# Performance work log

Hardware: AMD Instinct MI355X
Metric: run time of the kernel (lower is better)

## Reference

```python
import jax, jax.numpy as jnp
import numpy as np

EPS = 1e-06
K = 32


def setup_inputs() -> dict:
    key = jax.random.key(0)
    k1, k2, k3, k4, k5 = jax.random.split(key, 5)
    d_model, n_latents = 1024, 16384
    x = jax.random.normal(k1, (2, 2048, d_model), dtype=jnp.float32)
    b_pre = jax.random.normal(k2, (d_model,), dtype=jnp.float32) * 0.02
    W_enc = jax.random.normal(k3, (n_latents, d_model), dtype=jnp.float32) / np.sqrt(d_model)
    b_enc = jax.random.normal(k4, (n_latents,), dtype=jnp.float32) * 0.02
    W_dec = jax.random.normal(k5, (d_model, n_latents), dtype=jnp.float32)
    # mimic normalize_decoder_weights: unit norm along dim=1 (n_latents axis per row)
    W_dec = W_dec / jnp.linalg.norm(W_dec, axis=1, keepdims=True)
    return {"x": x, "b_pre": b_pre, "W_enc": W_enc, "b_enc": b_enc, "W_dec": W_dec}


def reference(x, b_pre, W_enc, b_enc, W_dec):
    B, S, D = x.shape
    # preprocess: center + normalize (torch .std is unbiased, ddof=1)
    mean = jnp.mean(x, axis=-1, keepdims=True)
    norm = jnp.std(x, axis=-1, keepdims=True, ddof=1) + EPS
    xn = ((x - mean) / norm).reshape(-1, D)          # [N, D]
    # encode
    h = (xn - b_pre) @ W_enc.T + b_enc               # [N, n_latents]
    # top-k + relu + scatter into sparse latent
    vals, idx = jax.lax.top_k(h, K)                  # [N, K]
    vals = jax.nn.relu(vals)
    rows = jnp.arange(h.shape[0])[:, None]
    h_sparse = jnp.zeros_like(h).at[rows, idx].set(vals)
    # decode (dense matmul over mostly-zero latents, as in the original)
    recon = h_sparse @ W_dec.T + b_pre               # [N, D]
    # postprocess: denormalize
    recon = recon.reshape(B, S, D) * norm + mean
    return recon
```

## Files before the change

### kernel.cpp

```cpp
#include <hip/hip_runtime.h>
#include <cstdint>
#include <cstddef>

typedef _Float16 half_t;
typedef _Float16 half4_t __attribute__((ext_vector_type(4)));
typedef _Float16 half8_t __attribute__((ext_vector_type(8)));
typedef unsigned short ushort8_t __attribute__((ext_vector_type(8)));
typedef float floatx4 __attribute__((ext_vector_type(4)));

#define NROWS 4096
#define DMODEL 1024
#define NLAT 16384
#define CAND_MAX 256

#define MBYTE (1ull << 20)
static const size_t oW0    = 0;
static const size_t oWdT   = 32 * MBYTE;
static const size_t oMeanF = 64 * MBYTE;
static const size_t oNormF = 64 * MBYTE + (64ull << 10);
static const size_t oMeanD = 64 * MBYTE + (128ull << 10);
static const size_t oNormD = 64 * MBYTE + (192ull << 10);
static const size_t oCandC = 64 * MBYTE + (256ull << 10);
static const size_t oCandI = 65 * MBYTE;
static const size_t oCandV = 69 * MBYTE;
static const size_t oBatch = 77 * MBYTE;

#define BATCH_ROW_BYTES 34816ull

__device__ __forceinline__ void gload16(const void* g, void* l) {
  __builtin_amdgcn_global_load_lds(
      (const __attribute__((address_space(1))) void*)g,
      (__attribute__((address_space(3))) void*)l, 16, 0, 0);
}

__device__ __forceinline__ uint32_t okey16(uint32_t u) {
  return (u & 0x8000u) ? ((~u) & 0xFFFFu) : (u | 0x8000u);
}
__device__ __forceinline__ float inv_okey16(uint32_t k) {
  unsigned short u = (k & 0x8000u) ? (unsigned short)(k & 0x7FFFu)
                                   : (unsigned short)(~k);
  return (float)__builtin_bit_cast(_Float16, u);
}

#define WSPLIT_B 2048
#define TRANS_B  4096
__global__ __launch_bounds__(256) void prepro_kernel(
    const float* __restrict__ x, const float* __restrict__ b_pre,
    const float* __restrict__ W_enc, const float* __restrict__ Wd,
    half_t* __restrict__ W0h, half_t* __restrict__ WdT,
    half_t* __restrict__ X0,
    float* __restrict__ meanF, float* __restrict__ normF,
    double* __restrict__ meanD, double* __restrict__ normD, int r0) {
  int bid = blockIdx.x, tid = threadIdx.x;
  if (bid < WSPLIT_B) {
    size_t base = (size_t)bid * 2048 + tid;
    for (int it = 0; it < 8; ++it) {
      size_t i = base + (size_t)it * 256;
      float4 v = ((const float4*)W_enc)[i];
      half4_t h0;
      h0[0] = (half_t)(v.x * 1024.0f);
      h0[1] = (half_t)(v.y * 1024.0f);
      h0[2] = (half_t)(v.z * 1024.0f);
      h0[3] = (half_t)(v.w * 1024.0f);
      ((half4_t*)W0h)[i] = h0;
    }
    return;
  }
  if (bid < WSPLIT_B + TRANS_B) {
    __shared__ float tile[64][65];
    int t = bid - WSPLIT_B;
    int c0 = (t & 255) * 64;
    int r0t = (t >> 8) * 64;
    int tc = tid & 63, tg = tid >> 6;
    for (int i = 0; i < 16; ++i) {
      int rr = i * 4 + tg;
      tile[rr][tc] = Wd[(size_t)(r0t + rr) * NLAT + c0 + tc];
    }
    __syncthreads();
    for (int i = 0; i < 16; ++i) {
      int cc = i * 4 + tg;
      WdT[(size_t)(c0 + cc) * DMODEL + r0t + tc] = (half_t)tile[tc][cc];
    }
    return;
  }
  int rl = bid - WSPLIT_B - TRANS_B;
  int rg = r0 + rl;
  const float4* px = (const float4*)(x + (size_t)rg * DMODEL);
  float4 v = px[tid];
  double s  = (double)v.x + (double)v.y + (double)v.z + (double)v.w;
  double sq = (double)v.x * v.x + (double)v.y * v.y +
              (double)v.z * v.z + (double)v.w * v.w;
  for (int off = 32; off; off >>= 1) {
    s += __shfl_down(s, off);
    sq += __shfl_down(sq, off);
  }
  __shared__ double ss[4], ssq[4];
  __shared__ double sMean, sNorm;
  int wv = tid >> 6, ln = tid & 63;
  if (ln == 0) { ss[wv] = s; ssq[wv] = sq; }
  __syncthreads();
  if (tid == 0) {
    double S = ss[0] + ss[1] + ss[2] + ss[3];
    double Q = ssq[0] + ssq[1] + ssq[2] + ssq[3];
    double mean = S / (double)DMODEL;
    double var = (Q - (double)DMODEL * mean * mean) / (double)(DMODEL - 1);
    double nrm = sqrt(var) + 1e-6;
    sMean = mean; sNorm = nrm;
    meanF[rg] = (float)mean; normF[rg] = (float)nrm;
    meanD[rg] = mean;        normD[rg] = nrm;
  }
  __syncthreads();
  float mean = (float)sMean, nrm = (float)sNorm;
  const float4* pb = (const float4*)b_pre;
  float4 bp = pb[tid];
  float c[4];
  c[0] = ((v.x - mean) / nrm - bp.x) * 1024.0f;
  c[1] = ((v.y - mean) / nrm - bp.y) * 1024.0f;
  c[2] = ((v.z - mean) / nrm - bp.z) * 1024.0f;
  c[3] = ((v.w - mean) / nrm - bp.w) * 1024.0f;
  half4_t h0;
  for (int i = 0; i < 4; ++i) h0[i] = (half_t)c[i];
  ((half4_t*)(X0 + (size_t)rl * DMODEL))[tid] = h0;
}

__global__ __launch_bounds__(512, 2) void gemm_enc(
    const half_t* __restrict__ X0, const half_t* __restrict__ W0,
    const float* __restrict__ b_enc, half_t* __restrict__ h, int mtiles) {
  __shared__ __align__(16) half_t As[2][256 * 64];
  __shared__ __align__(16) half_t Bs[2][256 * 64];
  int tid = threadIdx.x;
  int lane = tid & 63, wave = tid >> 6;
  int wm = wave >> 2, wn = wave & 3;

  int bid = blockIdx.x;
  int xcd = bid & 7, q = bid >> 3;
  int bn = xcd * 8 + (q & 7);
  int bm = q >> 3;
  (void)mtiles;

  const char* Ag = (const char*)(X0 + (size_t)bm * 256 * DMODEL);
  const char* Bg = (const char*)(W0 + (size_t)bn * 256 * DMODEL);

  int srcSwz = ((lane & 7) ^ (lane >> 3)) << 4;
  int rowBase = wave * 8 + (lane >> 3);
  int ldsWOff = wave * 1024;

#define STG_A(b, kt, pr) { int colB = ((kt) & 15) * 128 + srcSwz;             \
    gload16(Ag + (size_t)((pr) * 64 + rowBase) * 2048 + colB,                 \
            (char*)As[b] + (pr) * 8192 + ldsWOff);                            \
    gload16(Ag + (size_t)(((pr) + 2) * 64 + rowBase) * 2048 + colB,           \
            (char*)As[b] + ((pr) + 2) * 8192 + ldsWOff); }
#define STG_B(b, kt, pr) { int colB = ((kt) & 15) * 128 + srcSwz;             \
    gload16(Bg + (size_t)((pr) * 64 + rowBase) * 2048 + colB,                 \
            (char*)Bs[b] + (pr) * 8192 + ldsWOff);                            \
    gload16(Bg + (size_t)(((pr) + 2) * 64 + rowBase) * 2048 + colB,           \
            (char*)Bs[b] + ((pr) + 2) * 8192 + ldsWOff); }

  floatx4 acc[8][4] = {};

  STG_B(0, 0, 0); STG_B(0, 0, 1); STG_A(0, 0, 0); STG_A(0, 0, 1);
  STG_B(1, 1, 0); STG_B(1, 1, 1); STG_A(1, 1, 0);
  asm volatile("s_waitcnt vmcnt(6)" ::: "memory");
  __builtin_amdgcn_sched_barrier(0);
  __builtin_amdgcn_s_barrier();

  int laneQ = (lane & 15) * 128 + (lane >> 4) * 16;
  int sxor = (lane & 7) << 4;
  int aRow = wm * 128 * 128;
  int bRow = wn * 64 * 128;

  half8_t bfr[2][4], afr[4];
  const char *Ab, *Bb;

#define LD_A(mh, kk) _Pragma("unroll") for (int t = 0; t < 4; ++t)            \
    afr[t] = *(const half8_t*)(Ab + ((aRow + ((mh) * 4 + t) * 2048 +          \
                                      (kk) * 64 + laneQ) ^ sxor));
#define LD_B(kk) _Pragma("unroll") for (int t = 0; t < 4; ++t)                \
    bfr[kk][t] = *(const half8_t*)(Bb + ((bRow + t * 2048 +                   \
                                          (kk) * 64 + laneQ) ^ sxor));
#define MM(mb, kk) __builtin_amdgcn_s_setprio(1);                             \
    _Pragma("unroll") for (int mi = 0; mi < 4; ++mi)                          \
    _Pragma("unroll") for (int ni = 0; ni < 4; ++ni)                          \
      acc[(mb) + mi][ni] = __builtin_amdgcn_mfma_f32_16x16x32_f16(            \
          afr[mi], bfr[kk][ni], acc[(mb) + mi][ni], 0, 0, 0);                 \
    __builtin_amdgcn_s_setprio(0);
#define BAR() __builtin_amdgcn_s_barrier()
#define LGKM0() { asm volatile("s_waitcnt lgkmcnt(0)" ::: "memory");          \
    __builtin_amdgcn_sched_barrier(0); }
#define VM6() { asm volatile("s_waitcnt vmcnt(6)" ::: "memory");              \
    __builtin_amdgcn_sched_barrier(0); }

#pragma unroll 1
  for (int i = 0; i < 8; ++i) {
    int t0 = 2 * i;
    Ab = (const char*)As[0]; Bb = (const char*)Bs[0];
    LD_B(0); LD_B(1); LD_A(0, 0);
    STG_A(1, t0 + 1, 1);
    BAR(); LGKM0(); MM(0, 0); BAR();
    LD_A(1, 0);
    STG_B(0, t0 + 2, 0);
    BAR(); LGKM0(); MM(4, 0); BAR();
    LD_A(0, 1);
    STG_B(0, t0 + 2, 1);
    BAR(); LGKM0(); MM(0, 1); BAR();
    LD_A(1, 1);
    STG_A(0, t0 + 2, 0);
    BAR(); LGKM0(); MM(4, 1);
    VM6();
    BAR();
    Ab = (const char*)As[1]; Bb = (const char*)Bs[1];
    LD_B(0); LD_B(1); LD_A(0, 0);
    STG_A(0, t0 + 2, 1);
    BAR(); LGKM0(); MM(0, 0); BAR();
    LD_A(1, 0);
    STG_B(1, t0 + 3, 0);
    BAR(); LGKM0(); MM(4, 0); BAR();
    LD_A(0, 1);
    STG_B(1, t0 + 3, 1);
    BAR(); LGKM0(); MM(0, 1); BAR();
    LD_A(1, 1);
    STG_A(1, t0 + 3, 0);
    BAR(); LGKM0(); MM(4, 1);
    VM6();
    BAR();
  }
#undef STG_A
#undef STG_B
#undef LD_A
#undef LD_B
#undef MM
#undef BAR
#undef LGKM0
#undef VM6

  const float scale = 0x1p-20f;
  int rowb = bm * 256 + wm * 128 + ((lane >> 4) * 4);
  int colb = bn * 256 + wn * 64 + (lane & 15);
  float be[4];
#pragma unroll
  for (int ni = 0; ni < 4; ++ni) be[ni] = b_enc[colb + ni * 16];
#pragma unroll
  for (int mi = 0; mi < 8; ++mi)
#pragma unroll
    for (int ni = 0; ni < 4; ++ni)
#pragma unroll
      for (int r = 0; r < 4; ++r)
        h[(size_t)(rowb + mi * 16 + r) * NLAT + colb + ni * 16] =
            (half_t)(acc[mi][ni][r] * scale + be[ni]);
}

__global__ __launch_bounds__(256) void cand_kernel(
    const half_t* __restrict__ h, int* __restrict__ candIdx,
    int* __restrict__ candCnt, int r0) {
  int rl = blockIdx.x, tid = threadIdx.x;
  int rg = r0 + rl;
  const ushort8_t* ph8 = (const ushort8_t*)(h + (size_t)rl * NLAT);
  __shared__ uint32_t hist[8192];
  __shared__ int chunkSum[256];
  __shared__ float sThresh;
  __shared__ int cCount;

  for (int i = tid; i < 8192; i += 256) hist[i] = 0;
  if (tid == 0) cCount = 0;
  __syncthreads();

  for (int i = 0; i < 8; ++i) {
    ushort8_t v = ph8[tid + i * 256];
#pragma unroll
    for (int e = 0; e < 8; ++e)
      atomicAdd(&hist[okey16((uint32_t)v[e]) >> 3], 1u);
  }
  __syncthreads();
  {
    int s = 0;
    for (int b = 0; b < 32; ++b) s += (int)hist[tid * 32 + b];
    chunkSum[tid] = s;
  }
  __syncthreads();
  if (tid == 0) {
    int cum = 0, cchunk = 255;
    for (; cchunk > 0; --cchunk) {
      if (cum + chunkSum[cchunk] >= 32) break;
      cum += chunkSum[cchunk];
    }
    int b = cchunk * 32 + 31;
    for (; b > 0; --b) {
      if (cum + (int)hist[b] >= 32) break;
      cum += (int)hist[b];
    }
    sThresh = inv_okey16((uint32_t)b << 3) - 0.02f;
  }
  __syncthreads();
  float thresh = sThresh;

  for (int i = 0; i < 8; ++i) {
    ushort8_t v = ph8[tid + i * 256];
#pragma unroll
    for (int e = 0; e < 8; ++e) {
      float f = (float)__builtin_bit_cast(_Float16, (unsigned short)v[e]);
      if (f >= thresh) {
        int j = (tid + i * 256) * 8 + e;
        int slot = atomicAdd(&cCount, 1);
        if (slot < CAND_MAX) candIdx[(size_t)rg * CAND_MAX + slot] = j;
      }
    }
  }
  __syncthreads();
  if (tid == 0) candCnt[rg] = (cCount < CAND_MAX) ? cCount : CAND_MAX;
}

__global__ __launch_bounds__(256) void refine_dot(
    const float* __restrict__ x, const float* __restrict__ b_pre,
    const float* __restrict__ W_enc, const float* __restrict__ b_enc,
    const double* __restrict__ meanD, const double* __restrict__ normD,
    const int* __restrict__ candIdx, const int* __restrict__ candCnt,
    double* __restrict__ candV, int r0) {
  int rg = r0 + blockIdx.x;
  int tid = threadIdx.x;
  int wv = tid >> 6, ln = tid & 63;
  double mean = meanD[rg], nrm = normD[rg];
  const float* px = x + (size_t)rg * DMODEL;
  double xr[16];
#pragma unroll
  for (int u = 0; u < 16; ++u)
    xr[u] = ((double)px[ln + u * 64] - mean) / nrm - (double)b_pre[ln + u * 64];
  int nc = candCnt[rg];
  const int* ci = candIdx + (size_t)rg * CAND_MAX;

  for (int c0 = wv * 4; c0 < nc; c0 += 16) {
    const float* wp[4];
#pragma unroll
    for (int q = 0; q < 4; ++q) {
      int c = c0 + q;
      int j = ci[c < nc ? c : (nc - 1)];
      wp[q] = W_enc + (size_t)j * DMODEL + ln;
    }
    double a0 = 0.0, a1 = 0.0, a2 = 0.0, a3 = 0.0;
#pragma unroll
    for (int u = 0; u < 16; ++u) {
      float w0 = wp[0][u * 64];
      float w1 = wp[1][u * 64];
      float w2 = wp[2][u * 64];
      float w3 = wp[3][u * 64];
      a0 += xr[u] * (double)w0;
      a1 += xr[u] * (double)w1;
      a2 += xr[u] * (double)w2;
      a3 += xr[u] * (double)w3;
    }
    double accq[4] = {a0, a1, a2, a3};
#pragma unroll
    for (int q = 0; q < 4; ++q) {
      double s = accq[q];
      for (int off = 32; off; off >>= 1) s += __shfl_down(s, off);
      int c = c0 + q;
      if (ln == 0 && c < nc) {
        int j = ci[c];
        candV[(size_t)rg * CAND_MAX + c] = s + (double)b_enc[j];
      }
    }
  }
}

__global__ __launch_bounds__(256) void sel_decode(
    const double* __restrict__ candV, const int* __restrict__ candIdx,
    const int* __restrict__ candCnt,
    const half_t* __restrict__ WdT, const float* __restrict__ b_pre,
    const float* __restrict__ meanF, const float* __restrict__ normF,
    float* __restrict__ out, int r0) {
  int rg = r0 + blockIdx.x, tid = threadIdx.x;
  __shared__ double cV[CAND_MAX];
  __shared__ int cI[CAND_MAX];
  __shared__ float sVal[32];
  __shared__ int sIdx[32];
  int nc = candCnt[rg];
  for (int c = tid; c < nc; c += 256) {
    cV[c] = candV[(size_t)rg * CAND_MAX + c];
    cI[c] = candIdx[(size_t)rg * CAND_MAX + c];
  }
  if (tid < 32) { sVal[tid] = 0.0f; sIdx[tid] = 0; }
  __syncthreads();
  for (int c = tid; c < nc; c += 256) {
    double v = cV[c];
    int ix = cI[c];
    int rank = 0;
    for (int o = 0; o < nc; ++o) {
      double vo = cV[o];
      int io = cI[o];
      rank += (vo > v || (vo == v && io < ix)) ? 1 : 0;
    }
    if (rank < 32) {
      sIdx[rank] = ix;
      sVal[rank] = (float)(v > 0.0 ? v : 0.0);
    }
  }
  __syncthreads();
  int d0 = tid * 4;
  float4 accv = {0.f, 0.f, 0.f, 0.f};
#pragma unroll 8
  for (int k = 0; k < 32; ++k) {
    float vk = sVal[k];
    const half4_t wv = *(const half4_t*)(WdT + (size_t)sIdx[k] * DMODEL + d0);
    accv.x += vk * (float)wv[0]; accv.y += vk * (float)wv[1];
    accv.z += vk * (float)wv[2]; accv.w += vk * (float)wv[3];
  }
  float4 bp = ((const float4*)b_pre)[tid];
  float nrm = normF[rg], mn = meanF[rg];
  float4 o;
  o.x = (accv.x + bp.x) * nrm + mn;
  o.y = (accv.y + bp.y) * nrm + mn;
  o.z = (accv.z + bp.z) * nrm + mn;
  o.w = (accv.w + bp.w) * nrm + mn;
  ((float4*)(out + (size_t)rg * DMODEL))[tid] = o;
}

extern "C" void kernel_launch(void* const* d_in, const int* in_sizes, int n_in,
                              void* d_out, int out_size, void* d_ws, size_t ws_size,
                              hipStream_t stream) {
  const float* x     = (const float*)d_in[0];
  const float* b_pre = (const float*)d_in[1];
  const float* W_enc = (const float*)d_in[2];
  const float* b_enc = (const float*)d_in[3];
  const float* W_dec = (const float*)d_in[4];
  float* out = (float*)d_out;
  char* ws = (char*)d_ws;

  int rowsB = NROWS;
  while (rowsB > 256) {
    size_t need = oBatch + (size_t)rowsB * BATCH_ROW_BYTES;
    if (need <= ws_size) break;
    rowsB >>= 1;
  }
  if (oBatch + (size_t)rowsB * BATCH_ROW_BYTES > ws_size) return;

  half_t* W0 = (half_t*)(ws + oW0);
  half_t* WdT = (half_t*)(ws + oWdT);
  float* meanF = (float*)(ws + oMeanF);
  float* normF = (float*)(ws + oNormF);
  double* meanD = (double*)(ws + oMeanD);
  double* normD = (double*)(ws + oNormD);
  int*   candCnt = (int*)(ws + oCandC);
  int*   candIdx = (int*)(ws + oCandI);
  double* candV  = (double*)(ws + oCandV);
  half_t* X0b  = (half_t*)(ws + oBatch);
  half_t* hb   = X0b + (size_t)rowsB * DMODEL;

  for (int r0 = 0; r0 < NROWS; r0 += rowsB) {
    hipLaunchKernelGGL(prepro_kernel,
                       dim3(WSPLIT_B + TRANS_B + rowsB), dim3(256), 0, stream,
                       x, b_pre, W_enc, W_dec, W0, WdT, X0b,
                       meanF, normF, meanD, normD, r0);
    int mtiles = rowsB / 256;
    hipLaunchKernelGGL(gemm_enc, dim3(mtiles * 64), dim3(512), 0, stream,
                       X0b, W0, b_enc, hb, mtiles);
    hipLaunchKernelGGL(cand_kernel, dim3(rowsB), dim3(256), 0, stream,
                       hb, candIdx, candCnt, r0);
    hipLaunchKernelGGL(refine_dot, dim3(rowsB), dim3(256), 0, stream,
                       x, b_pre, W_enc, b_enc, meanD, normD, candIdx, candCnt,
                       candV, r0);
    hipLaunchKernelGGL(sel_decode, dim3(rowsB), dim3(256), 0, stream,
                       candV, candIdx, candCnt, WdT, b_pre, meanF, normF, out, r0);
  }
}
```

Baseline: 372.7 us.

## Fuse candidate, refine and decode kernels; double-buffer A fragments in GEMM

Merges the candidate-selection, fp64 refine dot-product and top-k select/decode kernels into one per-row postproc kernel that keeps candidates in shared memory. This drops two launches and the global round-trips of candidate indices, values and counts. The encoder GEMM now loads A fragments into two register sets with partial lgkmcnt waits so LDS reads overlap MFMAs, and peels the last iteration to stop issuing out-of-range prefetches. The cost is more registers and shared memory per block, which may lower occupancy in the fused kernel and the GEMM.

```diff
diff --git a/kernel.cpp b/kernel.cpp
--- a/kernel.cpp
+++ b/kernel.cpp
@@ -16,14 +16,9 @@
 #define MBYTE (1ull << 20)
 static const size_t oW0    = 0;
 static const size_t oWdT   = 32 * MBYTE;
-static const size_t oMeanF = 64 * MBYTE;
-static const size_t oNormF = 64 * MBYTE + (64ull << 10);
-static const size_t oMeanD = 64 * MBYTE + (128ull << 10);
-static const size_t oNormD = 64 * MBYTE + (192ull << 10);
-static const size_t oCandC = 64 * MBYTE + (256ull << 10);
-static const size_t oCandI = 65 * MBYTE;
-static const size_t oCandV = 69 * MBYTE;
-static const size_t oBatch = 77 * MBYTE;
+static const size_t oMeanD = 64 * MBYTE;
+static const size_t oNormD = 64 * MBYTE + (64ull << 10);
+static const size_t oBatch = 65 * MBYTE;
 
 #define BATCH_ROW_BYTES 34816ull
 
@@ -49,7 +44,6 @@
     const float* __restrict__ W_enc, const float* __restrict__ Wd,
     half_t* __restrict__ W0h, half_t* __restrict__ WdT,
     half_t* __restrict__ X0,
-    float* __restrict__ meanF, float* __restrict__ normF,
     double* __restrict__ meanD, double* __restrict__ normD, int r0) {
   int bid = blockIdx.x, tid = threadIdx.x;
   if (bid < WSPLIT_B) {
@@ -106,8 +100,7 @@
     double var = (Q - (double)DMODEL * mean * mean) / (double)(DMODEL - 1);
     double nrm = sqrt(var) + 1e-6;
     sMean = mean; sNorm = nrm;
-    meanF[rg] = (float)mean; normF[rg] = (float)nrm;
-    meanD[rg] = mean;        normD[rg] = nrm;
+    meanD[rg] = mean; normD[rg] = nrm;
   }
   __syncthreads();
   float mean = (float)sMean, nrm = (float)sNorm;
@@ -169,69 +162,85 @@
   int aRow = wm * 128 * 128;
   int bRow = wn * 64 * 128;
 
-  half8_t bfr[2][4], afr[4];
+  half8_t bfr[2][4], afA[4], afB[4];
   const char *Ab, *Bb;
 
-#define LD_A(mh, kk) _Pragma("unroll") for (int t = 0; t < 4; ++t)            \
-    afr[t] = *(const half8_t*)(Ab + ((aRow + ((mh) * 4 + t) * 2048 +          \
-                                      (kk) * 64 + laneQ) ^ sxor));
 #define LD_B(kk) _Pragma("unroll") for (int t = 0; t < 4; ++t)                \
     bfr[kk][t] = *(const half8_t*)(Bb + ((bRow + t * 2048 +                   \
                                           (kk) * 64 + laneQ) ^ sxor));
-#define MM(mb, kk) __builtin_amdgcn_s_setprio(1);                             \
+#define LD_AF(DST, mh, kk) _Pragma("unroll") for (int t = 0; t < 4; ++t)      \
+    DST[t] = *(const half8_t*)(Ab + ((aRow + ((mh) * 4 + t) * 2048 +          \
+                                      (kk) * 64 + laneQ) ^ sxor));
+#define MM(mb, FR, kk) __builtin_amdgcn_s_setprio(1);                         \
     _Pragma("unroll") for (int mi = 0; mi < 4; ++mi)                          \
     _Pragma("unroll") for (int ni = 0; ni < 4; ++ni)                          \
       acc[(mb) + mi][ni] = __builtin_amdgcn_mfma_f32_16x16x32_f16(            \
-          afr[mi], bfr[kk][ni], acc[(mb) + mi][ni], 0, 0, 0);                 \
+          FR[mi], bfr[kk][ni], acc[(mb) + mi][ni], 0, 0, 0);                  \
     __builtin_amdgcn_s_setprio(0);
 #define BAR() __builtin_amdgcn_s_barrier()
-#define LGKM0() { asm volatile("s_waitcnt lgkmcnt(0)" ::: "memory");          \
+#define LGKM(n) { asm volatile("s_waitcnt lgkmcnt(" #n ")" ::: "memory");     \
     __builtin_amdgcn_sched_barrier(0); }
 #define VM6() { asm volatile("s_waitcnt vmcnt(6)" ::: "memory");              \
     __builtin_amdgcn_sched_barrier(0); }
+#define VM0() { asm volatile("s_waitcnt vmcnt(0)" ::: "memory");              \
+    __builtin_amdgcn_sched_barrier(0); }
 
 #pragma unroll 1
-  for (int i = 0; i < 8; ++i) {
+  for (int i = 0; i < 7; ++i) {
     int t0 = 2 * i;
     Ab = (const char*)As[0]; Bb = (const char*)Bs[0];
-    LD_B(0); LD_B(1); LD_A(0, 0);
+    LD_B(0); LD_B(1); LD_AF(afA, 0, 0); LD_AF(afB, 1, 0);
     STG_A(1, t0 + 1, 1);
-    BAR(); LGKM0(); MM(0, 0); BAR();
-    LD_A(1, 0);
+    BAR(); LGKM(4); MM(0, afA, 0); BAR();
+    LD_AF(afA, 0, 1);
     STG_B(0, t0 + 2, 0);
-    BAR(); LGKM0(); MM(4, 0); BAR();
-    LD_A(0, 1);
+    BAR(); LGKM(4); MM(4, afB, 0); BAR();
+    LD_AF(afB, 1, 1);
     STG_B(0, t0 + 2, 1);
-    BAR(); LGKM0(); MM(0, 1); BAR();
-    LD_A(1, 1);
+    BAR(); LGKM(4); MM(0, afA, 1); BAR();
     STG_A(0, t0 + 2, 0);
-    BAR(); LGKM0(); MM(4, 1);
-    VM6();
-    BAR();
+    BAR(); LGKM(0); MM(4, afB, 1); VM6(); BAR();
     Ab = (const char*)As[1]; Bb = (const char*)Bs[1];
-    LD_B(0); LD_B(1); LD_A(0, 0);
+    LD_B(0); LD_B(1); LD_AF(afA, 0, 0); LD_AF(afB, 1, 0);
     STG_A(0, t0 + 2, 1);
-    BAR(); LGKM0(); MM(0, 0); BAR();
-    LD_A(1, 0);
+    BAR(); LGKM(4); MM(0, afA, 0); BAR();
+    LD_AF(afA, 0, 1);
     STG_B(1, t0 + 3, 0);
-    BAR(); LGKM0(); MM(4, 0); BAR();
-    LD_A(0, 1);
+    BAR(); LGKM(4); MM(4, afB, 0); BAR();
+    LD_AF(afB, 1, 1);
     STG_B(1, t0 + 3, 1);
-    BAR(); LGKM0(); MM(0, 1); BAR();
-    LD_A(1, 1);
+    BAR(); LGKM(4); MM(0, afA, 1); BAR();
     STG_A(1, t0 + 3, 0);
-    BAR(); LGKM0(); MM(4, 1);
-    VM6();
-    BAR();
+    BAR(); LGKM(0); MM(4, afB, 1); VM6(); BAR();
+  }
+  {
+    Ab = (const char*)As[0]; Bb = (const char*)Bs[0];
+    LD_B(0); LD_B(1); LD_AF(afA, 0, 0); LD_AF(afB, 1, 0);
+    STG_A(1, 15, 1);
+    BAR(); LGKM(4); MM(0, afA, 0); BAR();
+    LD_AF(afA, 0, 1);
+    BAR(); LGKM(4); MM(4, afB, 0); BAR();
+    LD_AF(afB, 1, 1);
+    BAR(); LGKM(4); MM(0, afA, 1); BAR();
+    BAR(); LGKM(0); MM(4, afB, 1); VM0(); BAR();
+    Ab = (const char*)As[1]; Bb = (const char*)Bs[1];
+    LD_B(0); LD_B(1); LD_AF(afA, 0, 0); LD_AF(afB, 1, 0);
+    LGKM(4); MM(0, afA, 0);
+    LD_AF(afA, 0, 1);
+    LGKM(4); MM(4, afB, 0);
+    LD_AF(afB, 1, 1);
+    LGKM(4); MM(0, afA, 1);
+    LGKM(0); MM(4, afB, 1);
   }
 #undef STG_A
 #undef STG_B
-#undef LD_A
 #undef LD_B
+#undef LD_AF
 #undef MM
 #undef BAR
-#undef LGKM0
+#undef LGKM
 #undef VM6
+#undef VM0
 
   const float scale = 0x1p-20f;
   int rowb = bm * 256 + wm * 128 + ((lane >> 4) * 4);
@@ -249,21 +258,36 @@
             (half_t)(acc[mi][ni][r] * scale + be[ni]);
 }
 
-__global__ __launch_bounds__(256) void cand_kernel(
-    const half_t* __restrict__ h, int* __restrict__ candIdx,
-    int* __restrict__ candCnt, int r0) {
+__global__ __launch_bounds__(256) void postproc(
+    const half_t* __restrict__ h, const float* __restrict__ x,
+    const float* __restrict__ b_pre, const float* __restrict__ W_enc,
+    const float* __restrict__ b_enc,
+    const double* __restrict__ meanD, const double* __restrict__ normD,
+    const half_t* __restrict__ WdT, float* __restrict__ out, int r0) {
   int rl = blockIdx.x, tid = threadIdx.x;
   int rg = r0 + rl;
+  int wv = tid >> 6, ln = tid & 63;
   const ushort8_t* ph8 = (const ushort8_t*)(h + (size_t)rl * NLAT);
+
   __shared__ uint32_t hist[8192];
   __shared__ int chunkSum[256];
   __shared__ float sThresh;
   __shared__ int cCount;
+  __shared__ int cI[CAND_MAX];
+  __shared__ double cV[CAND_MAX];
+  __shared__ float sVal[32];
+  __shared__ int sIdx[32];
+
+  double mean = meanD[rg], nrm = normD[rg];
+  const float* px = x + (size_t)rg * DMODEL;
+  double xr[16];
+#pragma unroll
+  for (int u = 0; u < 16; ++u)
+    xr[u] = ((double)px[ln + u * 64] - mean) / nrm - (double)b_pre[ln + u * 64];
 
   for (int i = tid; i < 8192; i += 256) hist[i] = 0;
   if (tid == 0) cCount = 0;
   __syncthreads();
-
   for (int i = 0; i < 8; ++i) {
     ushort8_t v = ph8[tid + i * 256];
 #pragma unroll
@@ -299,41 +323,21 @@
     for (int e = 0; e < 8; ++e) {
       float f = (float)__builtin_bit_cast(_Float16, (unsigned short)v[e]);
       if (f >= thresh) {
-        int j = (tid + i * 256) * 8 + e;
         int slot = atomicAdd(&cCount, 1);
-        if (slot < CAND_MAX) candIdx[(size_t)rg * CAND_MAX + slot] = j;
+        if (slot < CAND_MAX) cI[slot] = (tid + i * 256) * 8 + e;
       }
     }
   }
   __syncthreads();
-  if (tid == 0) candCnt[rg] = (cCount < CAND_MAX) ? cCount : CAND_MAX;
-}
-
-__global__ __launch_bounds__(256) void refine_dot(
-    const float* __restrict__ x, const float* __restrict__ b_pre,
-    const float* __restrict__ W_enc, const float* __restrict__ b_enc,
-    const double* __restrict__ meanD, const double* __restrict__ normD,
-    const int* __restrict__ candIdx, const int* __restrict__ candCnt,
-    double* __restrict__ candV, int r0) {
-  int rg = r0 + blockIdx.x;
-  int tid = threadIdx.x;
-  int wv = tid >> 6, ln = tid & 63;
-  double mean = meanD[rg], nrm = normD[rg];
-  const float* px = x + (size_t)rg * DMODEL;
-  double xr[16];
-#pragma unroll
-  for (int u = 0; u < 16; ++u)
-    xr[u] = ((double)px[ln + u * 64] - mean) / nrm - (double)b_pre[ln + u * 64];
-  int nc = candCnt[rg];
-  const int* ci = candIdx + (size_t)rg * CAND_MAX;
+  int nc = (cCount < CAND_MAX) ? cCount : CAND_MAX;
 
   for (int c0 = wv * 4; c0 < nc; c0 += 16) {
     const float* wp[4];
 #pragma unroll
-    for (int q = 0; q < 4; ++q) {
-      int c = c0 + q;
-      int j = ci[c < nc ? c : (nc - 1)];
-      wp[q] = W_enc + (size_t)j * DMODEL + ln;
+    for (int qq = 0; qq < 4; ++qq) {
+      int c = c0 + qq;
+      int j = cI[c < nc ? c : (nc - 1)];
+      wp[qq] = W_enc + (size_t)j * DMODEL + ln;
     }
     double a0 = 0.0, a1 = 0.0, a2 = 0.0, a3 = 0.0;
 #pragma unroll
@@ -349,36 +353,16 @@
     }
     double accq[4] = {a0, a1, a2, a3};
 #pragma unroll
-    for (int q = 0; q < 4; ++q) {
-      double s = accq[q];
+    for (int qq = 0; qq < 4; ++qq) {
+      double s = accq[qq];
       for (int off = 32; off; off >>= 1) s += __shfl_down(s, off);
-      int c = c0 + q;
-      if (ln == 0 && c < nc) {
-        int j = ci[c];
-        candV[(size_t)rg * CAND_MAX + c] = s + (double)b_enc[j];
-      }
-    }
-  }
-}
-
-__global__ __launch_bounds__(256) void sel_decode(
-    const double* __restrict__ candV, const int* __restrict__ candIdx,
-    const int* __restrict__ candCnt,
-    const half_t* __restrict__ WdT, const float* __restrict__ b_pre,
-    const float* __restrict__ meanF, const float* __restrict__ normF,
-    float* __restrict__ out, int r0) {
-  int rg = r0 + blockIdx.x, tid = threadIdx.x;
-  __shared__ double cV[CAND_MAX];
-  __shared__ int cI[CAND_MAX];
-  __shared__ float sVal[32];
-  __shared__ int sIdx[32];
-  int nc = candCnt[rg];
-  for (int c = tid; c < nc; c += 256) {
-    cV[c] = candV[(size_t)rg * CAND_MAX + c];
-    cI[c] = candIdx[(size_t)rg * CAND_MAX + c];
+      int c = c0 + qq;
+      if (ln == 0 && c < nc) cV[c] = s + (double)b_enc[cI[c]];
+    }
   }
   if (tid < 32) { sVal[tid] = 0.0f; sIdx[tid] = 0; }
   __syncthreads();
+
   for (int c = tid; c < nc; c += 256) {
     double v = cV[c];
     int ix = cI[c];
@@ -394,22 +378,23 @@
     }
   }
   __syncthreads();
+
   int d0 = tid * 4;
   float4 accv = {0.f, 0.f, 0.f, 0.f};
 #pragma unroll 8
   for (int k = 0; k < 32; ++k) {
     float vk = sVal[k];
-    const half4_t wv = *(const half4_t*)(WdT + (size_t)sIdx[k] * DMODEL + d0);
-    accv.x += vk * (float)wv[0]; accv.y += vk * (float)wv[1];
-    accv.z += vk * (float)wv[2]; accv.w += vk * (float)wv[3];
+    const half4_t wvv = *(const half4_t*)(WdT + (size_t)sIdx[k] * DMODEL + d0);
+    accv.x += vk * (float)wvv[0]; accv.y += vk * (float)wvv[1];
+    accv.z += vk * (float)wvv[2]; accv.w += vk * (float)wvv[3];
   }
   float4 bp = ((const float4*)b_pre)[tid];
-  float nrm = normF[rg], mn = meanF[rg];
+  float nrmf = (float)nrm, mnf = (float)mean;
   float4 o;
-  o.x = (accv.x + bp.x) * nrm + mn;
-  o.y = (accv.y + bp.y) * nrm + mn;
-  o.z = (accv.z + bp.z) * nrm + mn;
-  o.w = (accv.w + bp.w) * nrm + mn;
+  o.x = (accv.x + bp.x) * nrmf + mnf;
+  o.y = (accv.y + bp.y) * nrmf + mnf;
+  o.z = (accv.z + bp.z) * nrmf + mnf;
+  o.w = (accv.w + bp.w) * nrmf + mnf;
   ((float4*)(out + (size_t)rg * DMODEL))[tid] = o;
 }
 
@@ -434,30 +419,19 @@
 
   half_t* W0 = (half_t*)(ws + oW0);
   half_t* WdT = (half_t*)(ws + oWdT);
-  float* meanF = (float*)(ws + oMeanF);
-  float* normF = (float*)(ws + oNormF);
   double* meanD = (double*)(ws + oMeanD);
   double* normD = (double*)(ws + oNormD);
-  int*   candCnt = (int*)(ws + oCandC);
-  int*   candIdx = (int*)(ws + oCandI);
-  double* candV  = (double*)(ws + oCandV);
   half_t* X0b  = (half_t*)(ws + oBatch);
   half_t* hb   = X0b + (size_t)rowsB * DMODEL;
 
   for (int r0 = 0; r0 < NROWS; r0 += rowsB) {
     hipLaunchKernelGGL(prepro_kernel,
                        dim3(WSPLIT_B + TRANS_B + rowsB), dim3(256), 0, stream,
-                       x, b_pre, W_enc, W_dec, W0, WdT, X0b,
-                       meanF, normF, meanD, normD, r0);
+                       x, b_pre, W_enc, W_dec, W0, WdT, X0b, meanD, normD, r0);
     int mtiles = rowsB / 256;
     hipLaunchKernelGGL(gemm_enc, dim3(mtiles * 64), dim3(512), 0, stream,
                        X0b, W0, b_enc, hb, mtiles);
-    hipLaunchKernelGGL(cand_kernel, dim3(rowsB), dim3(256), 0, stream,
-                       hb, candIdx, candCnt, r0);
-    hipLaunchKernelGGL(refine_dot, dim3(rowsB), dim3(256), 0, stream,
-                       x, b_pre, W_enc, b_enc, meanD, normD, candIdx, candCnt,
-                       candV, r0);
-    hipLaunchKernelGGL(sel_decode, dim3(rowsB), dim3(256), 0, stream,
-                       candV, candIdx, candCnt, WdT, b_pre, meanF, normF, out, r0);
-  }
-}
+    hipLaunchKernelGGL(postproc, dim3(rowsB), dim3(256), 0, stream,
+                       hb, x, b_pre, W_enc, b_enc, meanD, normD, WdT, out, r0);
+  }
+}
```

After: 352.0 us. 5.5% less time.
